# Kernel tuning notes

Hardware: AMD Instinct MI355X
Metric: run time of the kernel (lower is better)

The kernel has to match this reference:

```python
import jax, jax.numpy as jnp
import numpy as np

# Phi-2 prefill geometry
B, S = 4, 1024            # 4 packed sequences of length 1024 (cu_seqlen_prefill path)
T = B * S                 # total flat tokens
H = 32                    # num_attention_heads
D = 80                    # head_size = hidden // heads
HID = H * D               # 2560
ROT = 32                  # rotary_dim = partial_rotary_factor(0.4) * head_size
HALF = ROT // 2
ROPE_THETA = 10000.0
SOFTMAX_SCALE = D ** -0.5


def setup_inputs() -> dict:
    key = jax.random.key(0)
    k0, k1, k2, k3, k4 = jax.random.split(key, 5)
    hidden_states = jax.random.normal(k0, (T, HID), dtype=jnp.float32)
    # positions restart per sequence (equal-length packed prefill)
    pos = jnp.tile(jnp.arange(S, dtype=jnp.float32), B)              # [T]
    inv_freq = 1.0 / (ROPE_THETA ** (jnp.arange(0, ROT, 2, dtype=jnp.float32) / ROT))  # [HALF]
    freqs = pos[:, None] * inv_freq[None, :]                         # [T, HALF]
    cos = jnp.cos(freqs)
    sin = jnp.sin(freqs)
    w_qkv = jax.random.normal(k1, (HID + 2 * HID, HID), dtype=jnp.float32) * 0.02
    b_qkv = jax.random.normal(k2, (HID + 2 * HID,), dtype=jnp.float32) * 0.02
    w_dense = jax.random.normal(k3, (HID, HID), dtype=jnp.float32) * 0.02
    b_dense = jax.random.normal(k4, (HID,), dtype=jnp.float32) * 0.02
    return {"hidden_states": hidden_states, "cos": cos, "sin": sin,
            "w_qkv": w_qkv, "b_qkv": b_qkv, "w_dense": w_dense, "b_dense": b_dense}


def _apply_partial_rotary(x, cos, sin):
    # x: [T, h, D]; rotate first ROT dims, GPT-NeoX half-split style (as in
    # lorax PositionRotaryEmbedding); remaining D-ROT dims pass through.
    x1 = x[..., :HALF]
    x2 = x[..., HALF:ROT]
    x_pass = x[..., ROT:]
    c = cos[:, None, :]  # [T,1,HALF]
    s = sin[:, None, :]
    o1 = x1 * c - x2 * s
    o2 = x2 * c + x1 * s
    return jnp.concatenate([o1, o2, x_pass], axis=-1)


def reference(hidden_states, cos, sin, w_qkv, b_qkv, w_dense, b_dense):
    # fused QKV projection (torch Linear: x @ W.T + b)
    qkv = hidden_states @ w_qkv.T + b_qkv                  # [T, 3*HID]
    q = qkv[:, :HID].reshape(T, H, D)
    k = qkv[:, HID:2 * HID].reshape(T, H, D)
    v = qkv[:, 2 * HID:].reshape(T, H, D)
    # rotary applied to query and key (key = kv[:,0]) before cache write
    q = _apply_partial_rotary(q, cos, sin)
    k = _apply_partial_rotary(k, cos, sin)
    # flash_attn prefill == varlen causal attention; equal-length packing
    # lets us batch it as [B,S,H,D]
    qb = q.reshape(B, S, H, D)
    kb = k.reshape(B, S, H, D)
    vb = v.reshape(B, S, H, D)
    scores = jnp.einsum("bqhd,bkhd->bhqk", qb, kb) * SOFTMAX_SCALE  # [B,H,S,S]
    causal = jnp.tril(jnp.ones((S, S), dtype=bool))
    scores = jnp.where(causal[None, None], scores, jnp.finfo(scores.dtype).min)
    attn = jax.nn.softmax(scores, axis=-1)
    out = jnp.einsum("bhqk,bkhd->bqhd", attn, vb)          # [B,S,H,D]
    out = out.reshape(T, HID)
    return out @ w_dense.T + b_dense                        # [T, HID]
```

## Files before the change

### kernel.cpp

```cpp
#include <hip/hip_runtime.h>

typedef __attribute__((ext_vector_type(8))) __bf16 bf16x8;
typedef __attribute__((ext_vector_type(4))) float f32x4;

#define NH 32
#define DH 80
#define SEQ 1024
#define NB 4
#define NT 4096
#define HID 2560
#define NQKV 7680
#define SM_SCALE 0.11180339887498948f

static __device__ __forceinline__ unsigned short f2bf(float f) {
  unsigned u = __builtin_bit_cast(unsigned, f);
  u += 0x7fffu + ((u >> 16) & 1u);
  return (unsigned short)(u >> 16);
}
static __device__ __forceinline__ float bf2f(unsigned short s) {
  unsigned u = (unsigned)s << 16;
  return __builtin_bit_cast(float, u);
}

typedef __attribute__((address_space(1))) const unsigned int as1_uint;
typedef __attribute__((address_space(3))) unsigned int as3_uint;
static __device__ __forceinline__ void gload16(const void* g, void* l) {
  __builtin_amdgcn_global_load_lds((as1_uint*)g, (as3_uint*)l, 16, 0, 0);
}

__global__ __launch_bounds__(256) void cvt_kernel(const float* __restrict__ in,
                                                  unsigned short* __restrict__ out,
                                                  int n4) {
  const float4* __restrict__ in4 = (const float4*)in;
  ushort4* __restrict__ out4 = (ushort4*)out;
  for (int i = blockIdx.x * blockDim.x + threadIdx.x; i < n4;
       i += gridDim.x * blockDim.x) {
    float4 v = in4[i];
    ushort4 o;
    o.x = f2bf(v.x);
    o.y = f2bf(v.y);
    o.z = f2bf(v.z);
    o.w = f2bf(v.w);
    out4[i] = o;
  }
}

template <int EPI>
__global__ __launch_bounds__(512, 2) void gemm8p_kernel(
    const unsigned short* __restrict__ A, const unsigned short* __restrict__ Bm,
    const float* __restrict__ bias, unsigned short* __restrict__ Cq,
    unsigned short* __restrict__ Ck, unsigned short* __restrict__ Cv,
    float* __restrict__ Cf, int M, int N, int K) {
  __shared__ __align__(16) unsigned short AL[2][2][8192];
  __shared__ __align__(16) unsigned short BL[2][2][8192];
  const int tid = threadIdx.x;
  const int lane = tid & 63, w = tid >> 6;
  const int wm = w >> 2, wn = w & 3;
  const int lr = lane & 15, lg = lane >> 4;
  const int bhh = wn >> 1;
  const int brow = (wn & 1) * 64;

  const int gx = gridDim.x;
  const int nwg = gx * gridDim.y;
  int bid = blockIdx.y * gx + blockIdx.x;
  bid = (bid & 7) * (nwg >> 3) + (bid >> 3);
  const int n0 = (bid % gx) * 256;
  const int m0 = (bid / gx) * 256;

  const unsigned short* asrc[2][2];
  const unsigned short* bsrc[2][2];
#pragma unroll
  for (int h = 0; h < 2; ++h)
#pragma unroll
    for (int j = 0; j < 2; ++j) {
      const int off = j * 8192 + tid * 16;
      const int u = off ^ (((off >> 7) & 7) << 4);
      const int row = u >> 7, col = (u & 127) >> 1;
      asrc[h][j] = A + (size_t)(m0 + h * 128 + row) * K + col;
      bsrc[h][j] = Bm + (size_t)(n0 + h * 128 + row) * K + col;
    }

  const int NK = K >> 6, NIT = NK >> 1;

#define SA(buf, h, kt)                                                     \
  do {                                                                     \
    gload16(asrc[h][0] + (size_t)(kt) * 64,                                \
            (char*)&AL[buf][h][0] + w * 1024);                             \
    gload16(asrc[h][1] + (size_t)(kt) * 64,                                \
            (char*)&AL[buf][h][0] + 8192 + w * 1024);                      \
  } while (0)
#define SB(buf, h, kt)                                                     \
  do {                                                                     \
    gload16(bsrc[h][0] + (size_t)(kt) * 64,                                \
            (char*)&BL[buf][h][0] + w * 1024);                             \
    gload16(bsrc[h][1] + (size_t)(kt) * 64,                                \
            (char*)&BL[buf][h][0] + 8192 + w * 1024);                      \
  } while (0)
#define FA(buf, lrow, ks)                                                  \
  (*(const bf16x8*)((const char*)&AL[buf][wm][0] +                         \
                    (((lrow) * 128 + (ks) * 64 + lg * 16) ^                \
                     (((lrow) & 7) << 4))))
#define FB(buf, lrow, ks)                                                  \
  (*(const bf16x8*)((const char*)&BL[buf][bhh][0] +                        \
                    (((lrow) * 128 + (ks) * 64 + lg * 16) ^                \
                     (((lrow) & 7) << 4))))
#define PH_MFMA(AIDX, NBASE, BREG)                                         \
  __builtin_amdgcn_s_barrier();                                            \
  __builtin_amdgcn_s_setprio(1);                                           \
  _Pragma("unroll") for (int mf = 0; mf < 4; ++mf)                         \
      _Pragma("unroll") for (int nf = 0; nf < 2; ++nf) {                   \
    acc[AIDX + mf][NBASE + nf] = __builtin_amdgcn_mfma_f32_16x16x32_bf16(  \
        af[mf * 2 + 0], BREG[nf * 2 + 0], acc[AIDX + mf][NBASE + nf], 0, 0, 0); \
    acc[AIDX + mf][NBASE + nf] = __builtin_amdgcn_mfma_f32_16x16x32_bf16(  \
        af[mf * 2 + 1], BREG[nf * 2 + 1], acc[AIDX + mf][NBASE + nf], 0, 0, 0); \
  }                                                                        \
  __builtin_amdgcn_s_setprio(0);

  f32x4 acc[8][4];
#pragma unroll
  for (int i = 0; i < 8; ++i)
#pragma unroll
    for (int j = 0; j < 4; ++j) acc[i][j] = (f32x4)0.0f;

  SB(0, 0, 0); SA(0, 0, 0); SB(0, 1, 0); SA(0, 1, 0);
  SB(1, 0, 1); SA(1, 0, 1);
  asm volatile("s_waitcnt vmcnt(4)" ::: "memory");
  __builtin_amdgcn_s_barrier();

  bf16x8 af[8], bl[4], bhf[4];

  for (int i = 0; i < NIT; ++i) {
    const int t1 = 2 * i + 1, t2 = 2 * i + 2, t3 = 2 * i + 3;
    const bool p2 = t2 < NK, p3 = t3 < NK;

#pragma unroll
    for (int mf = 0; mf < 4; ++mf) {
      af[mf * 2 + 0] = FA(0, mf * 16 + lr, 0);
      af[mf * 2 + 1] = FA(0, mf * 16 + lr, 1);
    }
#pragma unroll
    for (int nf = 0; nf < 2; ++nf) {
      bl[nf * 2 + 0] = FB(0, brow + nf * 16 + lr, 0);
      bl[nf * 2 + 1] = FB(0, brow + nf * 16 + lr, 1);
    }
    SB(1, 1, t1);
    PH_MFMA(0, 0, bl)
    __builtin_amdgcn_s_barrier();
#pragma unroll
    for (int nf = 0; nf < 2; ++nf) {
      bhf[nf * 2 + 0] = FB(0, brow + (nf + 2) * 16 + lr, 0);
      bhf[nf * 2 + 1] = FB(0, brow + (nf + 2) * 16 + lr, 1);
    }
    SA(1, 1, t1);
    PH_MFMA(0, 2, bhf)
    __builtin_amdgcn_s_barrier();
#pragma unroll
    for (int mf = 0; mf < 4; ++mf) {
      af[mf * 2 + 0] = FA(0, 64 + mf * 16 + lr, 0);
      af[mf * 2 + 1] = FA(0, 64 + mf * 16 + lr, 1);
    }
    if (p2) SB(0, 0, t2);
    PH_MFMA(4, 0, bl)
    __builtin_amdgcn_s_barrier();
    if (p2) SA(0, 0, t2);
    PH_MFMA(4, 2, bhf)
    if (i + 1 < NIT)
      asm volatile("s_waitcnt vmcnt(4)" ::: "memory");
    else
      asm volatile("s_waitcnt vmcnt(0)" ::: "memory");
    __builtin_amdgcn_s_barrier();

#pragma unroll
    for (int mf = 0; mf < 4; ++mf) {
      af[mf * 2 + 0] = FA(1, mf * 16 + lr, 0);
      af[mf * 2 + 1] = FA(1, mf * 16 + lr, 1);
    }
#pragma unroll
    for (int nf = 0; nf < 2; ++nf) {
      bl[nf * 2 + 0] = FB(1, brow + nf * 16 + lr, 0);
      bl[nf * 2 + 1] = FB(1, brow + nf * 16 + lr, 1);
    }
    if (p2) SB(0, 1, t2);
    PH_MFMA(0, 0, bl)
    __builtin_amdgcn_s_barrier();
#pragma unroll
    for (int nf = 0; nf < 2; ++nf) {
      bhf[nf * 2 + 0] = FB(1, brow + (nf + 2) * 16 + lr, 0);
      bhf[nf * 2 + 1] = FB(1, brow + (nf + 2) * 16 + lr, 1);
    }
    if (p2) SA(0, 1, t2);
    PH_MFMA(0, 2, bhf)
    __builtin_amdgcn_s_barrier();
#pragma unroll
    for (int mf = 0; mf < 4; ++mf) {
      af[mf * 2 + 0] = FA(1, 64 + mf * 16 + lr, 0);
      af[mf * 2 + 1] = FA(1, 64 + mf * 16 + lr, 1);
    }
    if (p3) SB(1, 0, t3);
    PH_MFMA(4, 0, bl)
    __builtin_amdgcn_s_barrier();
    if (p3) SA(1, 0, t3);
    PH_MFMA(4, 2, bhf)
    if (i + 1 < NIT) asm volatile("s_waitcnt vmcnt(4)" ::: "memory");
    __builtin_amdgcn_s_barrier();
  }
#undef SA
#undef SB
#undef FA
#undef FB
#undef PH_MFMA

  if (EPI == 0) {
    if (n0 >= 2 * HID) {
      unsigned short* scr = (unsigned short*)&AL[0][0][0] + w * 2176;
      const int bb = (m0 + wm * 128) >> 10;
      const int ssb = (m0 + wm * 128) & 1023;
#pragma unroll
      for (int nf = 0; nf < 4; ++nf) {
        const int col0 = n0 - 2 * HID + wn * 64 + nf * 16;
        const int hh = col0 / DH;
        const int dd0 = col0 - hh * DH;
        const float bv = bias[2 * HID + col0 + lr];
#pragma unroll
        for (int mf = 0; mf < 8; ++mf) {
          ushort4 p;
          p.x = f2bf(acc[mf][nf][0] + bv);
          p.y = f2bf(acc[mf][nf][1] + bv);
          p.z = f2bf(acc[mf][nf][2] + bv);
          p.w = f2bf(acc[mf][nf][3] + bv);
          *(ushort4*)&scr[lr * 136 + mf * 16 + lg * 4] = p;
        }
#pragma unroll
        for (int it = 0; it < 4; ++it) {
          const int dd = (lane >> 4) + it * 4;
          const int sl = (lane & 15) * 8;
          bf16x8 v = *(const bf16x8*)&scr[dd * 136 + sl];
          *(bf16x8*)(Cv + ((size_t)(bb * NH + hh) * DH + dd0 + dd) * SEQ + ssb + sl) = v;
        }
        asm volatile("s_waitcnt lgkmcnt(0)" ::: "memory");
      }
    } else {
#pragma unroll
      for (int nf = 0; nf < 4; ++nf) {
        const int col = n0 + wn * 64 + nf * 16 + lr;
        const int sec = col >= HID ? 1 : 0;
        const int rem = col - sec * HID;
        const int hh = rem / DH;
        const int dd = rem - hh * DH;
        unsigned short* dst = sec ? Ck : Cq;
        const float bv = bias[col];
#pragma unroll
        for (int mf = 0; mf < 8; ++mf) {
#pragma unroll
          for (int r = 0; r < 4; ++r) {
            const int tr = m0 + wm * 128 + mf * 16 + lg * 4 + r;
            const int bb2 = tr >> 10, ss = tr & 1023;
            dst[((size_t)(bb2 * NH + hh) * SEQ + ss) * DH + dd] =
                f2bf(acc[mf][nf][r] + bv);
          }
        }
      }
    }
  } else {
#pragma unroll
    for (int nf = 0; nf < 4; ++nf) {
      const int col = n0 + wn * 64 + nf * 16 + lr;
      const float bv = bias[col];
#pragma unroll
      for (int mf = 0; mf < 8; ++mf)
#pragma unroll
        for (int r = 0; r < 4; ++r) {
          const int row = m0 + wm * 128 + mf * 16 + lg * 4 + r;
          Cf[row * N + col] = acc[mf][nf][r] + bv;
        }
    }
  }
}

__global__ __launch_bounds__(256) void rope_kernel(unsigned short* __restrict__ Q,
                                                   unsigned short* __restrict__ K,
                                                   const float* __restrict__ cosb,
                                                   const float* __restrict__ sinb) {
  const int idx = blockIdx.x * 256 + threadIdx.x;
  const int i = idx & 15;
  const int s = (idx >> 4) & 1023;
  const int bh = idx >> 14;
  const int b = bh >> 5;
  const int t = b * SEQ + s;
  const float c = cosb[t * 16 + i];
  const float sn = sinb[t * 16 + i];
  const int base = (bh * SEQ + s) * DH;
  float q1 = bf2f(Q[base + i]), q2 = bf2f(Q[base + 16 + i]);
  Q[base + i] = f2bf(q1 * c - q2 * sn);
  Q[base + 16 + i] = f2bf(q2 * c + q1 * sn);
  float k1 = bf2f(K[base + i]), k2 = bf2f(K[base + 16 + i]);
  K[base + i] = f2bf(k1 * c - k2 * sn);
  K[base + 16 + i] = f2bf(k2 * c + k1 * sn);
}

__global__ __launch_bounds__(512) void attn_kernel(const unsigned short* __restrict__ Qb,
                                                   const unsigned short* __restrict__ Kb,
                                                   const unsigned short* __restrict__ Vg,
                                                   unsigned short* __restrict__ Ob) {
  __shared__ __align__(16) unsigned short Klds[64][104];
  __shared__ __align__(16) unsigned short Vt[80][72];
  __shared__ __align__(16) unsigned short Plds[8][32][72];
  const int tid = threadIdx.x;
  const int lane = tid & 63, w = tid >> 6;
  const int lr = lane & 15, lg = lane >> 4;
  const int koff = lg * 8;
  const int qt = blockIdx.x, bh = blockIdx.y;
  const int h = bh & 31;
  const int base = bh * (SEQ * DH);
  const int vbase = bh * (DH * SEQ);

  for (int e = tid; e < 64 * 16; e += 512) Klds[e >> 4][80 + (e & 15)] = 0;

  const int rowbase = qt * 256 + w * 32;
  bf16x8 qf[2][3];
#pragma unroll
  for (int hh = 0; hh < 2; ++hh)
#pragma unroll
    for (int c = 0; c < 3; ++c) {
      const int d = c * 32 + koff;
      if (d < DH)
        qf[hh][c] =
            *(const bf16x8*)(Qb + base + (rowbase + hh * 16 + lr) * DH + d);
      else
        qf[hh][c] = (bf16x8)(__bf16)0.0f;
    }

  float m[2][4], l[2][4];
  f32x4 of[2][5];
#pragma unroll
  for (int hh = 0; hh < 2; ++hh) {
#pragma unroll
    for (int r = 0; r < 4; ++r) {
      m[hh][r] = -3.0e38f;
      l[hh][r] = 0.0f;
    }
#pragma unroll
    for (int d = 0; d < 5; ++d) of[hh][d] = (f32x4)0.0f;
  }

  const int ke0r = tid / 10, ke0c = (tid - (tid / 10) * 10) * 8;
  const int ke1 = tid + 512;
  const int ke1r = ke1 / 10, ke1c = (ke1 - (ke1 / 10) * 10) * 8;
  const int ve0d = tid >> 3, ve0c = (tid & 7) * 8;
  const int ve1d = (tid + 512) >> 3, ve1c = ((tid + 512) & 7) * 8;

  bf16x8 kreg0, kreg1, vreg0, vreg1;
  kreg0 = *(const bf16x8*)(Kb + base + ke0r * DH + ke0c);
  if (tid < 128) kreg1 = *(const bf16x8*)(Kb + base + ke1r * DH + ke1c);
  vreg0 = *(const bf16x8*)(Vg + vbase + ve0d * SEQ + ve0c);
  if (tid < 128) vreg1 = *(const bf16x8*)(Vg + vbase + ve1d * SEQ + ve1c);

  const int ktmax = 4 * qt + 3;
  for (int kt = 0; kt <= ktmax; ++kt) {
    __syncthreads();
    *(bf16x8*)&Klds[ke0r][ke0c] = kreg0;
    if (tid < 128) *(bf16x8*)&Klds[ke1r][ke1c] = kreg1;
    *(bf16x8*)&Vt[ve0d][ve0c] = vreg0;
    if (tid < 128) *(bf16x8*)&Vt[ve1d][ve1c] = vreg1;
    __syncthreads();

    if (kt < ktmax) {
      const int nb = (kt + 1) * 64;
      kreg0 = *(const bf16x8*)(Kb + base + (nb + ke0r) * DH + ke0c);
      if (tid < 128) kreg1 = *(const bf16x8*)(Kb + base + (nb + ke1r) * DH + ke1c);
      vreg0 = *(const bf16x8*)(Vg + vbase + ve0d * SEQ + nb + ve0c);
      if (tid < 128) vreg1 = *(const bf16x8*)(Vg + vbase + ve1d * SEQ + nb + ve1c);
    }

    if (kt * 64 > rowbase + 31) continue;

    f32x4 sc[2][4];
#pragma unroll
    for (int hh = 0; hh < 2; ++hh)
#pragma unroll
      for (int cf = 0; cf < 4; ++cf) sc[hh][cf] = (f32x4)0.0f;
#pragma unroll
    for (int c = 0; c < 3; ++c) {
#pragma unroll
      for (int cf = 0; cf < 4; ++cf) {
        bf16x8 kb = *(const bf16x8*)&Klds[cf * 16 + lr][c * 32 + koff];
        sc[0][cf] = __builtin_amdgcn_mfma_f32_16x16x32_bf16(qf[0][c], kb, sc[0][cf], 0, 0, 0);
        sc[1][cf] = __builtin_amdgcn_mfma_f32_16x16x32_bf16(qf[1][c], kb, sc[1][cf], 0, 0, 0);
      }
    }

#pragma unroll
    for (int hh = 0; hh < 2; ++hh) {
      const int rowg = rowbase + hh * 16 + lg * 4;
#pragma unroll
      for (int cf = 0; cf < 4; ++cf) {
        const int colg = kt * 64 + cf * 16 + lr;
#pragma unroll
        for (int r = 0; r < 4; ++r) {
          float v = sc[hh][cf][r] * SM_SCALE;
          if (colg > rowg + r) v = -1.0e30f;
          sc[hh][cf][r] = v;
        }
      }
      float al[4];
#pragma unroll
      for (int r = 0; r < 4; ++r) {
        float mx = fmaxf(fmaxf(sc[hh][0][r], sc[hh][1][r]),
                         fmaxf(sc[hh][2][r], sc[hh][3][r]));
#pragma unroll
        for (int off = 1; off < 16; off <<= 1) mx = fmaxf(mx, __shfl_xor(mx, off, 64));
        const float mnew = fmaxf(m[hh][r], mx);
        al[r] = __expf(m[hh][r] - mnew);
        m[hh][r] = mnew;
      }
      float ls[4] = {0.f, 0.f, 0.f, 0.f};
#pragma unroll
      for (int cf = 0; cf < 4; ++cf)
#pragma unroll
        for (int r = 0; r < 4; ++r) {
          const float p = __expf(sc[hh][cf][r] - m[hh][r]);
          sc[hh][cf][r] = p;
          ls[r] += p;
        }
#pragma unroll
      for (int r = 0; r < 4; ++r) {
        float sv = ls[r];
#pragma unroll
        for (int off = 1; off < 16; off <<= 1) sv += __shfl_xor(sv, off, 64);
        l[hh][r] = l[hh][r] * al[r] + sv;
      }
#pragma unroll
      for (int d = 0; d < 5; ++d)
#pragma unroll
        for (int r = 0; r < 4; ++r) of[hh][d][r] *= al[r];
#pragma unroll
      for (int cf = 0; cf < 4; ++cf)
#pragma unroll
        for (int r = 0; r < 4; ++r)
          Plds[w][hh * 16 + lg * 4 + r][cf * 16 + lr] = f2bf(sc[hh][cf][r]);
    }

#pragma unroll
    for (int kc = 0; kc < 2; ++kc) {
      bf16x8 pa0 = *(const bf16x8*)&Plds[w][lr][kc * 32 + koff];
      bf16x8 pa1 = *(const bf16x8*)&Plds[w][16 + lr][kc * 32 + koff];
#pragma unroll
      for (int d = 0; d < 5; ++d) {
        bf16x8 vb = *(const bf16x8*)&Vt[d * 16 + lr][kc * 32 + koff];
        of[0][d] = __builtin_amdgcn_mfma_f32_16x16x32_bf16(pa0, vb, of[0][d], 0, 0, 0);
        of[1][d] = __builtin_amdgcn_mfma_f32_16x16x32_bf16(pa1, vb, of[1][d], 0, 0, 0);
      }
    }
  }

#pragma unroll
  for (int hh = 0; hh < 2; ++hh) {
    const int t = (bh >> 5) * SEQ + rowbase + hh * 16 + lg * 4;
#pragma unroll
    for (int r = 0; r < 4; ++r) {
      const float rl = 1.0f / l[hh][r];
#pragma unroll
      for (int d = 0; d < 5; ++d)
        Ob[(t + r) * HID + h * DH + d * 16 + lr] = f2bf(of[hh][d][r] * rl);
    }
  }
}

extern "C" void kernel_launch(void* const* d_in, const int* in_sizes, int n_in,
                              void* d_out, int out_size, void* d_ws, size_t ws_size,
                              hipStream_t stream) {
  const float* hs = (const float*)d_in[0];
  const float* cosb = (const float*)d_in[1];
  const float* sinb = (const float*)d_in[2];
  const float* w_qkv = (const float*)d_in[3];
  const float* b_qkv = (const float*)d_in[4];
  const float* w_dense = (const float*)d_in[5];
  const float* b_dense = (const float*)d_in[6];
  float* out = (float*)d_out;
  char* ws = (char*)d_ws;

  unsigned short* hsb = (unsigned short*)(ws + 0);
  unsigned short* aob = (unsigned short*)(ws + 0);
  unsigned short* wqb = (unsigned short*)(ws + 20971520);
  unsigned short* wdb = (unsigned short*)(ws + 20971520);
  unsigned short* Qb = (unsigned short*)(ws + 60293120);
  unsigned short* Kb = (unsigned short*)(ws + 81264640);
  unsigned short* Vb = (unsigned short*)(ws + 102236160);

  cvt_kernel<<<2048, 256, 0, stream>>>(hs, hsb, (NT * HID) / 4);
  cvt_kernel<<<2048, 256, 0, stream>>>(w_qkv, wqb, (NQKV * HID) / 4);
  gemm8p_kernel<0><<<dim3(NQKV / 256, NT / 256), 512, 0, stream>>>(
      hsb, wqb, b_qkv, Qb, Kb, Vb, nullptr, NT, NQKV, HID);
  cvt_kernel<<<2048, 256, 0, stream>>>(w_dense, wdb, (HID * HID) / 4);
  rope_kernel<<<(NB * NH * SEQ * 16) / 256, 256, 0, stream>>>(Qb, Kb, cosb, sinb);
  attn_kernel<<<dim3(SEQ / 256, NB * NH), 512, 0, stream>>>(Qb, Kb, Vb, aob);
  gemm8p_kernel<1><<<dim3(HID / 256, NT / 256), 512, 0, stream>>>(
      aob, wdb, b_dense, nullptr, nullptr, nullptr, out, NT, HID, HID);
}
```

Before: 412.4 us.

## Batch GEMM stage prefetches, fold softmax scale into Q, skip lazy rescale

The GEMM main loop now issues both halves of each next stage's A/B loads together and waits at vmcnt(8) instead of interleaving single loads. This deepens the outstanding-load window and lowers barrier coupling, at the cost of holding more loads in flight. In attention, the softmax scale is applied to Q once in the rope kernel, and causal masking is skipped for fully visible tiles. Online-softmax rescaling of the output and row sum is now done only when the running max grows by more than a threshold (lazy rescale), which removes exp and multiply work but lets un-normalised values grow further.

```diff
diff --git a/kernel.cpp b/kernel.cpp
--- a/kernel.cpp
+++ b/kernel.cpp
@@ -122,16 +122,16 @@
 #pragma unroll
     for (int j = 0; j < 4; ++j) acc[i][j] = (f32x4)0.0f;
 
-  SB(0, 0, 0); SA(0, 0, 0); SB(0, 1, 0); SA(0, 1, 0);
-  SB(1, 0, 1); SA(1, 0, 1);
-  asm volatile("s_waitcnt vmcnt(4)" ::: "memory");
+  SB(0, 0, 0); SB(0, 1, 0); SA(0, 0, 0); SA(0, 1, 0);
+  SB(1, 0, 1); SB(1, 1, 1); SA(1, 0, 1); SA(1, 1, 1);
+  asm volatile("s_waitcnt vmcnt(8)" ::: "memory");
   __builtin_amdgcn_s_barrier();
 
   bf16x8 af[8], bl[4], bhf[4];
 
   for (int i = 0; i < NIT; ++i) {
-    const int t1 = 2 * i + 1, t2 = 2 * i + 2, t3 = 2 * i + 3;
-    const bool p2 = t2 < NK, p3 = t3 < NK;
+    const int t2 = 2 * i + 2, t3 = 2 * i + 3;
+    const bool pf = (i + 1) < NIT;
 
 #pragma unroll
     for (int mf = 0; mf < 4; ++mf) {
@@ -143,7 +143,6 @@
       bl[nf * 2 + 0] = FB(0, brow + nf * 16 + lr, 0);
       bl[nf * 2 + 1] = FB(0, brow + nf * 16 + lr, 1);
     }
-    SB(1, 1, t1);
     PH_MFMA(0, 0, bl)
     __builtin_amdgcn_s_barrier();
 #pragma unroll
@@ -151,7 +150,6 @@
       bhf[nf * 2 + 0] = FB(0, brow + (nf + 2) * 16 + lr, 0);
       bhf[nf * 2 + 1] = FB(0, brow + (nf + 2) * 16 + lr, 1);
     }
-    SA(1, 1, t1);
     PH_MFMA(0, 2, bhf)
     __builtin_amdgcn_s_barrier();
 #pragma unroll
@@ -159,13 +157,13 @@
       af[mf * 2 + 0] = FA(0, 64 + mf * 16 + lr, 0);
       af[mf * 2 + 1] = FA(0, 64 + mf * 16 + lr, 1);
     }
-    if (p2) SB(0, 0, t2);
+    if (pf) { SB(0, 0, t2); SB(0, 1, t2); }
     PH_MFMA(4, 0, bl)
     __builtin_amdgcn_s_barrier();
-    if (p2) SA(0, 0, t2);
+    if (pf) { SA(0, 0, t2); SA(0, 1, t2); }
     PH_MFMA(4, 2, bhf)
-    if (i + 1 < NIT)
-      asm volatile("s_waitcnt vmcnt(4)" ::: "memory");
+    if (pf)
+      asm volatile("s_waitcnt vmcnt(8)" ::: "memory");
     else
       asm volatile("s_waitcnt vmcnt(0)" ::: "memory");
     __builtin_amdgcn_s_barrier();
@@ -180,7 +178,6 @@
       bl[nf * 2 + 0] = FB(1, brow + nf * 16 + lr, 0);
       bl[nf * 2 + 1] = FB(1, brow + nf * 16 + lr, 1);
     }
-    if (p2) SB(0, 1, t2);
     PH_MFMA(0, 0, bl)
     __builtin_amdgcn_s_barrier();
 #pragma unroll
@@ -188,7 +185,6 @@
       bhf[nf * 2 + 0] = FB(1, brow + (nf + 2) * 16 + lr, 0);
       bhf[nf * 2 + 1] = FB(1, brow + (nf + 2) * 16 + lr, 1);
     }
-    if (p2) SA(0, 1, t2);
     PH_MFMA(0, 2, bhf)
     __builtin_amdgcn_s_barrier();
 #pragma unroll
@@ -196,12 +192,12 @@
       af[mf * 2 + 0] = FA(1, 64 + mf * 16 + lr, 0);
       af[mf * 2 + 1] = FA(1, 64 + mf * 16 + lr, 1);
     }
-    if (p3) SB(1, 0, t3);
+    if (pf) { SB(1, 0, t3); SB(1, 1, t3); }
     PH_MFMA(4, 0, bl)
     __builtin_amdgcn_s_barrier();
-    if (p3) SA(1, 0, t3);
+    if (pf) { SA(1, 0, t3); SA(1, 1, t3); }
     PH_MFMA(4, 2, bhf)
-    if (i + 1 < NIT) asm volatile("s_waitcnt vmcnt(4)" ::: "memory");
+    if (pf) asm volatile("s_waitcnt vmcnt(8)" ::: "memory");
     __builtin_amdgcn_s_barrier();
   }
 #undef SA
@@ -291,8 +287,13 @@
   const float sn = sinb[t * 16 + i];
   const int base = (bh * SEQ + s) * DH;
   float q1 = bf2f(Q[base + i]), q2 = bf2f(Q[base + 16 + i]);
-  Q[base + i] = f2bf(q1 * c - q2 * sn);
-  Q[base + 16 + i] = f2bf(q2 * c + q1 * sn);
+  Q[base + i] = f2bf((q1 * c - q2 * sn) * SM_SCALE);
+  Q[base + 16 + i] = f2bf((q2 * c + q1 * sn) * SM_SCALE);
+#pragma unroll
+  for (int j = 0; j < 3; ++j) {
+    const int d = 32 + j * 16 + i;
+    Q[base + d] = f2bf(bf2f(Q[base + d]) * SM_SCALE);
+  }
   float k1 = bf2f(K[base + i]), k2 = bf2f(K[base + 16 + i]);
   K[base + i] = f2bf(k1 * c - k2 * sn);
   K[base + 16 + i] = f2bf(k2 * c + k1 * sn);
@@ -373,6 +374,7 @@
     }
 
     if (kt * 64 > rowbase + 31) continue;
+    const bool fullvis = (kt * 64 + 63 <= rowbase);
 
     f32x4 sc[2][4];
 #pragma unroll
@@ -391,27 +393,42 @@
 
 #pragma unroll
     for (int hh = 0; hh < 2; ++hh) {
-      const int rowg = rowbase + hh * 16 + lg * 4;
-#pragma unroll
-      for (int cf = 0; cf < 4; ++cf) {
-        const int colg = kt * 64 + cf * 16 + lr;
+      if (!fullvis) {
+        const int rowg = rowbase + hh * 16 + lg * 4;
+#pragma unroll
+        for (int cf = 0; cf < 4; ++cf) {
+          const int colg = kt * 64 + cf * 16 + lr;
+#pragma unroll
+          for (int r = 0; r < 4; ++r)
+            if (colg > rowg + r) sc[hh][cf][r] = -1.0e30f;
+        }
+      }
+      float mx[4];
+#pragma unroll
+      for (int r = 0; r < 4; ++r) {
+        float v = fmaxf(fmaxf(sc[hh][0][r], sc[hh][1][r]),
+                        fmaxf(sc[hh][2][r], sc[hh][3][r]));
+#pragma unroll
+        for (int off = 1; off < 16; off <<= 1) v = fmaxf(v, __shfl_xor(v, off, 64));
+        mx[r] = v;
+      }
+      bool need = false;
+#pragma unroll
+      for (int r = 0; r < 4; ++r) need |= (mx[r] > m[hh][r] + 8.0f);
+      if (__ballot(need)) {
+        float al[4];
 #pragma unroll
         for (int r = 0; r < 4; ++r) {
-          float v = sc[hh][cf][r] * SM_SCALE;
-          if (colg > rowg + r) v = -1.0e30f;
-          sc[hh][cf][r] = v;
-        }
-      }
-      float al[4];
-#pragma unroll
-      for (int r = 0; r < 4; ++r) {
-        float mx = fmaxf(fmaxf(sc[hh][0][r], sc[hh][1][r]),
-                         fmaxf(sc[hh][2][r], sc[hh][3][r]));
-#pragma unroll
-        for (int off = 1; off < 16; off <<= 1) mx = fmaxf(mx, __shfl_xor(mx, off, 64));
-        const float mnew = fmaxf(m[hh][r], mx);
-        al[r] = __expf(m[hh][r] - mnew);
-        m[hh][r] = mnew;
+          const float mn = fmaxf(m[hh][r], mx[r]);
+          al[r] = __expf(m[hh][r] - mn);
+          m[hh][r] = mn;
+        }
+#pragma unroll
+        for (int d = 0; d < 5; ++d)
+#pragma unroll
+          for (int r = 0; r < 4; ++r) of[hh][d][r] *= al[r];
+#pragma unroll
+        for (int r = 0; r < 4; ++r) l[hh][r] *= al[r];
       }
       float ls[4] = {0.f, 0.f, 0.f, 0.f};
 #pragma unroll
@@ -427,12 +444,8 @@
         float sv = ls[r];
 #pragma unroll
         for (int off = 1; off < 16; off <<= 1) sv += __shfl_xor(sv, off, 64);
-        l[hh][r] = l[hh][r] * al[r] + sv;
-      }
-#pragma unroll
-      for (int d = 0; d < 5; ++d)
-#pragma unroll
-        for (int r = 0; r < 4; ++r) of[hh][d][r] *= al[r];
+        l[hh][r] += sv;
+      }
 #pragma unroll
       for (int cf = 0; cf < 4; ++cf)
 #pragma unroll
```

New measurement: 398.6 us. -3.4%, faster.
